# Kernel tuning notes

Hardware: AMD Instinct MI355X
Metric: run time of the kernel (lower is better)

The kernel has to match this reference:

```python
import jax, jax.numpy as jnp
import numpy as np

H = 1024  # hidden_size
I = 1     # input_size / output_size


def _lstm_cell(x_t, h, c, Wih, Whh, b):
    # PyTorch gate order: i, f, g, o ; Wih:[4H,I], Whh:[4H,H], b:[4H]
    gates = x_t @ Wih.T + h @ Whh.T + b          # [B, 4H]
    i, f, g, o = jnp.split(gates, 4, axis=-1)
    c_new = jax.nn.sigmoid(f) * c + jax.nn.sigmoid(i) * jnp.tanh(g)
    h_new = jax.nn.sigmoid(o) * jnp.tanh(c_new)
    return h_new, c_new


def setup_inputs() -> dict:
    key = jax.random.key(0)
    ks = jax.random.split(key, 10)
    s = 1.0 / np.sqrt(H)
    u = lambda k, shp: jax.random.uniform(k, shp, jnp.float32, -s, s)
    seq_len, batch = 512, 512
    return {
        "x": jax.random.normal(ks[0], (seq_len, batch, I), jnp.float32),
        "enc_Wih": u(ks[1], (4 * H, I)),
        "enc_Whh": u(ks[2], (4 * H, H)),
        "enc_b": u(ks[3], (4 * H,)),
        "dec_Wih": u(ks[4], (4 * H, I)),
        "dec_Whh": u(ks[5], (4 * H, H)),
        "dec_b": u(ks[6], (4 * H,)),
        "lin_W": u(ks[7], (I, H)),
        "lin_b": u(ks[8], (I,)),
        "target_len": 64,
    }


def reference(x, enc_Wih, enc_Whh, enc_b, dec_Wih, dec_Whh, dec_b, lin_W, lin_b, target_len):
    batch = x.shape[1]
    h0 = jnp.zeros((batch, H), x.dtype)
    c0 = jnp.zeros((batch, H), x.dtype)

    # Encoder: single LSTM over the full sequence; only final (h, c) is used.
    def enc_step(carry, x_t):
        h, c = carry
        h, c = _lstm_cell(x_t, h, c, enc_Wih, enc_Whh, enc_b)
        return (h, c), None

    (h, c), _ = jax.lax.scan(enc_step, (h0, c0), x)

    # Recursive decoder: feed own output back as next input.
    def dec_step(carry, _):
        h, c, y_in = carry
        h, c = _lstm_cell(y_in, h, c, dec_Wih, dec_Whh, dec_b)
        y = h @ lin_W.T + lin_b                  # [B, I]
        return (h, c, y), y

    dec_in0 = x[-1]                              # [B, I]
    _, y = jax.lax.scan(dec_step, (h, c, dec_in0), None, length=target_len)
    return y                                      # [target_len, B, I]
```

## Files before the change

kernel.cpp:

```cpp
#include <hip/hip_runtime.h>
#include <cstdint>
#include <cstddef>


#define HD    1024
#define G4    4096
#define NSTEP 576
#define TLEN  64

typedef __bf16 bf16x8 __attribute__((ext_vector_type(8)));
typedef float  f32x4  __attribute__((ext_vector_type(4)));
typedef __attribute__((address_space(1))) const unsigned int glob_u32;
typedef __attribute__((address_space(3))) unsigned int lds_u32;

__device__ __forceinline__ unsigned short f2bf(float f) {
  unsigned u = __builtin_bit_cast(unsigned, f);
  u = u + 0x7FFFu + ((u >> 16) & 1u);
  return (unsigned short)(u >> 16);
}
__device__ __forceinline__ float bf2f(unsigned short h) {
  return __builtin_bit_cast(float, (unsigned)h << 16);
}
__device__ __forceinline__ float sigm(float x) { return 1.0f / (1.0f + __expf(-x)); }
__device__ __forceinline__ float tanh_(float x) { return 1.0f - 2.0f / (1.0f + __expf(2.0f * x)); }

__global__ __launch_bounds__(256) void prep_w(const float* __restrict__ Whh,
                                              const float* __restrict__ Wih,
                                              const float* __restrict__ linW,
                                              int fold,
                                              unsigned short* __restrict__ dst) {
  int gid  = blockIdx.x * 256 + threadIdx.x;
  int rowg = gid >> 8;
  int k0   = (gid & 255) << 2;
  float4 wv = *reinterpret_cast<const float4*>(Whh + (size_t)rowg * HD + k0);
  if (fold) {
    float wi = Wih[rowg];
    float4 lw = *reinterpret_cast<const float4*>(linW + k0);
    wv.x += wi * lw.x; wv.y += wi * lw.y; wv.z += wi * lw.z; wv.w += wi * lw.w;
  }
  ushort4 hi, lo;
  hi.x = f2bf(wv.x); lo.x = f2bf(wv.x - bf2f(hi.x));
  hi.y = f2bf(wv.y); lo.y = f2bf(wv.y - bf2f(hi.y));
  hi.z = f2bf(wv.z); lo.z = f2bf(wv.z - bf2f(hi.z));
  hi.w = f2bf(wv.w); lo.w = f2bf(wv.w - bf2f(hi.w));
  int g = rowg >> 10, j = rowg & 1023;
  int tile = j >> 3, c = g * 8 + (j & 7);
  size_t base = (size_t)tile * 65536 + (size_t)c * 1024 + (size_t)(k0 ^ ((c & 7) << 3));
  *reinterpret_cast<ushort4*>(dst + base)         = hi;
  *reinterpret_cast<ushort4*>(dst + base + 32768) = lo;
}

__global__ __launch_bounds__(256) void init_out(float* __restrict__ out,
                                                const float* __restrict__ lin_b) {
  int i = blockIdx.x * 256 + threadIdx.x;
  if (i < TLEN * 512) out[i] = lin_b[0];
}

__global__ __launch_bounds__(512, 1) void lstm_step(
    const float* __restrict__ xv,
    const float* __restrict__ psub,
    const float* __restrict__ xcp,
    const float* __restrict__ Wih,
    const float* __restrict__ bias,
    const float* __restrict__ linW,
    const unsigned short* __restrict__ wbuf,
    const unsigned short* __restrict__ hT_in,
    unsigned short* __restrict__ hT_out,
    float* __restrict__ c_buf,
    float* __restrict__ yout)
{
  __shared__ __align__(16) unsigned char smem[131072 + 512];
  const int tid  = threadIdx.x;
  const int lane = tid & 63;
  const int wid  = tid >> 6;
  const int l15  = lane & 15;
  const int lk   = lane >> 4;

  const int bid  = blockIdx.x;
  const int rh   = (bid >> 2) & 1;
  const int tile = (bid >> 3) * 4 + (bid & 3);

  {
    glob_u32* g = (glob_u32*)(wbuf + (size_t)tile * 65536);
    lds_u32*  l = (lds_u32*)smem;
#pragma unroll
    for (int i = 0; i < 16; ++i)
      __builtin_amdgcn_global_load_lds(g + i * 2048 + tid * 4,
                                       l + i * 2048 + tid * 4, 16, 0, 0);
  }
  float* wihs = (float*)(smem + 131072);
  float* bs   = (float*)(smem + 131072 + 128);
  float* lws  = (float*)(smem + 131072 + 256);
  if (tid < 32) {
    int g = tid >> 3, jj = tid & 7;
    int r = g * HD + tile * 8 + jj;
    wihs[tid] = Wih[r];
    bs[tid]   = bias[r];
  } else if (tid < 40) {
    lws[tid - 32] = linW[tile * 8 + (tid - 32)];
  }
  __syncthreads();

  const int rowbase = rh * 256 + wid * 32;
  const unsigned short* pa[2];
#pragma unroll
  for (int m = 0; m < 2; ++m)
    pa[m] = hT_in + (size_t)(rowbase + m * 16 + l15) * 32 + lk * 8;

  int QH[2], QL[2];
#pragma unroll
  for (int nt = 0; nt < 2; ++nt) {
    int c = nt * 16 + l15;
    int s = (c & 7) << 4;
    int q = c * 2048 + ((lk * 16) ^ s);
    QH[nt] = q;
    QL[nt] = 65536 + q;
  }

  f32x4 acc[2][2] = {};
  bf16x8 Af[3][2], BH[2][2], BL[2][2];

#define LOADA(kk, st)                                                        \
  { _Pragma("unroll") for (int m = 0; m < 2; ++m)                            \
      Af[st][m] = *(const bf16x8*)(pa[m] + (size_t)(kk) * 16384); }
#define LOADB(kk, st)                                                        \
  { _Pragma("unroll") for (int nt = 0; nt < 2; ++nt) {                       \
      BH[st][nt] = *(const bf16x8*)(smem + (QH[nt] ^ ((kk) << 6)));          \
      BL[st][nt] = *(const bf16x8*)(smem + (QL[nt] ^ ((kk) << 6))); } }

  LOADA(0, 0); LOADA(1, 1); LOADB(0, 0);
#pragma unroll
  for (int kk = 0; kk < 32; ++kk) {
    if (kk + 2 < 32) LOADA(kk + 2, (kk + 2) % 3);
    if (kk + 1 < 32) LOADB(kk + 1, (kk + 1) & 1);
#pragma unroll
    for (int m = 0; m < 2; ++m)
#pragma unroll
      for (int nt = 0; nt < 2; ++nt) {
        acc[m][nt] = __builtin_amdgcn_mfma_f32_16x16x32_bf16(
            Af[kk % 3][m], BH[kk & 1][nt], acc[m][nt], 0, 0, 0);
        acc[m][nt] = __builtin_amdgcn_mfma_f32_16x16x32_bf16(
            Af[kk % 3][m], BL[kk & 1][nt], acc[m][nt], 0, 0, 0);
      }
  }
#undef LOADA
#undef LOADB

  __syncthreads();
  float* gl = (float*)smem;
#pragma unroll
  for (int m = 0; m < 2; ++m)
#pragma unroll
    for (int nt = 0; nt < 2; ++nt)
#pragma unroll
      for (int r = 0; r < 4; ++r)
        gl[(wid * 32 + m * 16 + lk * 4 + r) * 33 + nt * 16 + l15] = acc[m][nt][r];
  __syncthreads();

  const int row  = tid >> 1;
  const int jp   = tid & 1;
  const int grow = rh * 256 + row;
  float xs = 0.0f;
  if (xv)   xs += xv[grow];
  if (psub) xs -= psub[grow];
  if (xcp)  xs += xcp[0];

  float* cp = c_buf + (size_t)tile * 4096 + rh * 2048 + row * 8 + jp * 4;
  float4 cold = *reinterpret_cast<const float4*>(cp);
  float4 cnew;
  ushort4 hw;
  float ypart = 0.0f;
#pragma unroll
  for (int q = 0; q < 4; ++q) {
    int jj = jp * 4 + q;
    float gi = gl[row * 33 + jj]      + xs * wihs[jj]      + bs[jj];
    float gf = gl[row * 33 + 8 + jj]  + xs * wihs[8 + jj]  + bs[8 + jj];
    float gg = gl[row * 33 + 16 + jj] + xs * wihs[16 + jj] + bs[16 + jj];
    float go = gl[row * 33 + 24 + jj] + xs * wihs[24 + jj] + bs[24 + jj];
    float cv = (&cold.x)[q];
    float cn = sigm(gf) * cv + sigm(gi) * tanh_(gg);
    float hn = sigm(go) * tanh_(cn);
    (&cnew.x)[q] = cn;
    ypart += hn * lws[jj];
    ((unsigned short*)&hw)[q] = f2bf(hn);
  }
  *reinterpret_cast<float4*>(cp) = cnew;
  const int kblk = tile >> 2;
  const int keb  = (tile & 3) * 8;
  *reinterpret_cast<ushort4*>(hT_out + (size_t)kblk * 16384 + (size_t)grow * 32
                              + keb + jp * 4) = hw;
  if (yout) {
    ypart += __shfl_xor(ypart, 1);
    if ((lane & 1) == 0) atomicAdd(yout + grow, ypart);
  }
}

extern "C" void kernel_launch(void* const* d_in, const int* in_sizes, int n_in,
                              void* d_out, int out_size, void* d_ws, size_t ws_size,
                              hipStream_t stream) {
  const float* x       = (const float*)d_in[0];
  const float* enc_Wih = (const float*)d_in[1];
  const float* enc_Whh = (const float*)d_in[2];
  const float* enc_b   = (const float*)d_in[3];
  const float* dec_Wih = (const float*)d_in[4];
  const float* dec_Whh = (const float*)d_in[5];
  const float* dec_b   = (const float*)d_in[6];
  const float* lin_W   = (const float*)d_in[7];
  const float* lin_b   = (const float*)d_in[8];
  float* out = (float*)d_out;

  uint8_t* w = (uint8_t*)d_ws;
  const size_t MB = 1u << 20;
  float*          c_buf = (float*)(w + 0 * MB);
  unsigned short* hT0   = (unsigned short*)(w + 2 * MB);
  float*          p     = (float*)(w + 3 * MB);
  unsigned short* hT1   = (unsigned short*)(w + 4 * MB);
  unsigned short* wenc  = (unsigned short*)(w + 8 * MB);
  unsigned short* wdec  = (unsigned short*)(w + 24 * MB);
  unsigned short* hT[2] = { hT0, hT1 };

  hipMemsetAsync(d_ws, 0, 3 * MB + 4096, stream);
  init_out<<<128, 256, 0, stream>>>(out, lin_b);
  prep_w<<<4096, 256, 0, stream>>>(enc_Whh, enc_Wih, lin_W, 0, wenc);
  prep_w<<<4096, 256, 0, stream>>>(dec_Whh, dec_Wih, lin_W, 1, wdec);

  for (int t = 0; t < NSTEP; ++t) {
    const unsigned short* hin = hT[t & 1];
    unsigned short* hout      = hT[(t + 1) & 1];
    if (t < 512) {
      lstm_step<<<256, 512, 0, stream>>>(
          x + (size_t)t * 512, nullptr, nullptr,
          enc_Wih, enc_b, lin_W, wenc, hin, hout, c_buf,
          (t == 511) ? p : nullptr);
    } else if (t == 512) {
      lstm_step<<<256, 512, 0, stream>>>(
          x + (size_t)511 * 512, p, nullptr,
          dec_Wih, dec_b, lin_W, wdec, hin, hout, c_buf, out);
    } else {
      int s = t - 512;
      lstm_step<<<256, 512, 0, stream>>>(
          nullptr, nullptr, lin_b,
          dec_Wih, dec_b, lin_W, wdec, hin, hout, c_buf,
          out + (size_t)s * 512);
    }
  }
  (void)in_sizes; (void)n_in; (void)out_size; (void)ws_size;
}
```

Baseline: 11.79 ms.

## Replace per-step kernel launches with a persistent kernel using grid barriers

```diff
diff --git a/kernel.cpp b/kernel.cpp
--- a/kernel.cpp
+++ b/kernel.cpp
@@ -56,20 +56,28 @@
   if (i < TLEN * 512) out[i] = lin_b[0];
 }
 
-__global__ __launch_bounds__(512, 1) void lstm_step(
-    const float* __restrict__ xv,
-    const float* __restrict__ psub,
-    const float* __restrict__ xcp,
-    const float* __restrict__ Wih,
-    const float* __restrict__ bias,
+__global__ __launch_bounds__(512, 1) void lstm_persist(
+    const float* __restrict__ x,
+    const float* __restrict__ enc_Wih,
+    const float* __restrict__ enc_b,
+    const float* __restrict__ dec_Wih,
+    const float* __restrict__ dec_b,
     const float* __restrict__ linW,
-    const unsigned short* __restrict__ wbuf,
-    const unsigned short* __restrict__ hT_in,
-    unsigned short* __restrict__ hT_out,
-    float* __restrict__ c_buf,
-    float* __restrict__ yout)
+    const float* __restrict__ linb_p,
+    const unsigned short* __restrict__ wenc,
+    const unsigned short* __restrict__ wdec,
+    unsigned short* __restrict__ hA,
+    unsigned short* __restrict__ hB,
+    float* __restrict__ p,
+    unsigned* __restrict__ bar,
+    float* __restrict__ out)
 {
-  __shared__ __align__(16) unsigned char smem[131072 + 512];
+  __shared__ __align__(16) unsigned char smem[148480];
+  float* gl   = (float*)(smem + 131072);
+  float* wihs = (float*)(smem + 131072 + 16896);
+  float* bs   = wihs + 32;
+  float* lws  = wihs + 64;
+
   const int tid  = threadIdx.x;
   const int lane = tid & 63;
   const int wid  = tid >> 6;
@@ -79,33 +87,15 @@
   const int bid  = blockIdx.x;
   const int rh   = (bid >> 2) & 1;
   const int tile = (bid >> 3) * 4 + (bid & 3);
-
-  {
-    glob_u32* g = (glob_u32*)(wbuf + (size_t)tile * 65536);
-    lds_u32*  l = (lds_u32*)smem;
-#pragma unroll
-    for (int i = 0; i < 16; ++i)
-      __builtin_amdgcn_global_load_lds(g + i * 2048 + tid * 4,
-                                       l + i * 2048 + tid * 4, 16, 0, 0);
-  }
-  float* wihs = (float*)(smem + 131072);
-  float* bs   = (float*)(smem + 131072 + 128);
-  float* lws  = (float*)(smem + 131072 + 256);
-  if (tid < 32) {
-    int g = tid >> 3, jj = tid & 7;
-    int r = g * HD + tile * 8 + jj;
-    wihs[tid] = Wih[r];
-    bs[tid]   = bias[r];
-  } else if (tid < 40) {
-    lws[tid - 32] = linW[tile * 8 + (tid - 32)];
-  }
-  __syncthreads();
+  const int kblk = tile >> 2;
+  const float linb = linb_p[0];
+  unsigned* cnt = bar + rh * 32;
 
   const int rowbase = rh * 256 + wid * 32;
-  const unsigned short* pa[2];
+  size_t aoff[2];
 #pragma unroll
   for (int m = 0; m < 2; ++m)
-    pa[m] = hT_in + (size_t)(rowbase + m * 16 + l15) * 32 + lk * 8;
+    aoff[m] = (size_t)(rowbase + m * 16 + l15) * 32 + (size_t)lk * 8;
 
   int QH[2], QL[2];
 #pragma unroll
@@ -117,8 +107,47 @@
     QL[nt] = 65536 + q;
   }
 
-  f32x4 acc[2][2] = {};
-  bf16x8 Af[3][2], BH[2][2], BL[2][2];
+  const int rowc = tid >> 2;
+  const int jq   = tid & 3;
+
+  float c_reg[2][2] = {{0.f, 0.f}, {0.f, 0.f}};
+
+#define STAGE(WB, WIH, BB)                                                   \
+  {                                                                          \
+    glob_u32* gsrc = (glob_u32*)((WB) + (size_t)tile * 65536);               \
+    lds_u32*  ldst = (lds_u32*)smem;                                         \
+    _Pragma("unroll")                                                        \
+    for (int i = 0; i < 16; ++i)                                             \
+      __builtin_amdgcn_global_load_lds(gsrc + i * 2048 + tid * 4,            \
+                                       ldst + i * 2048 + tid * 4, 16, 0, 0); \
+    if (tid < 32) {                                                          \
+      int gg = tid >> 3, jj = tid & 7;                                       \
+      int r = gg * HD + tile * 8 + jj;                                       \
+      wihs[tid] = (WIH)[r];                                                  \
+      bs[tid]   = (BB)[r];                                                   \
+    } else if (tid < 40) {                                                   \
+      lws[tid - 32] = linW[tile * 8 + (tid - 32)];                           \
+    }                                                                        \
+  }
+
+  STAGE(wenc, enc_Wih, enc_b);
+  __syncthreads();
+
+#pragma unroll 1
+  for (int t = 0; t < NSTEP; ++t) {
+    if (t == 512) {
+      STAGE(wdec, dec_Wih, dec_b);
+      __syncthreads();
+    }
+    const unsigned short* hin = (t & 1) ? hB : hA;
+    unsigned short* hout      = (t & 1) ? hA : hB;
+
+    const unsigned short* pa[2];
+#pragma unroll
+    for (int m = 0; m < 2; ++m) pa[m] = hin + aoff[m];
+
+    f32x4 acc[2][2] = {};
+    bf16x8 Af[3][2], BH[2][2], BL[2][2];
 
 #define LOADA(kk, st)                                                        \
   { _Pragma("unroll") for (int m = 0; m < 2; ++m)                            \
@@ -128,71 +157,83 @@
       BH[st][nt] = *(const bf16x8*)(smem + (QH[nt] ^ ((kk) << 6)));          \
       BL[st][nt] = *(const bf16x8*)(smem + (QL[nt] ^ ((kk) << 6))); } }
 
-  LOADA(0, 0); LOADA(1, 1); LOADB(0, 0);
-#pragma unroll
-  for (int kk = 0; kk < 32; ++kk) {
-    if (kk + 2 < 32) LOADA(kk + 2, (kk + 2) % 3);
-    if (kk + 1 < 32) LOADB(kk + 1, (kk + 1) & 1);
-#pragma unroll
-    for (int m = 0; m < 2; ++m)
-#pragma unroll
-      for (int nt = 0; nt < 2; ++nt) {
-        acc[m][nt] = __builtin_amdgcn_mfma_f32_16x16x32_bf16(
-            Af[kk % 3][m], BH[kk & 1][nt], acc[m][nt], 0, 0, 0);
-        acc[m][nt] = __builtin_amdgcn_mfma_f32_16x16x32_bf16(
-            Af[kk % 3][m], BL[kk & 1][nt], acc[m][nt], 0, 0, 0);
-      }
-  }
+    LOADA(0, 0); LOADA(1, 1); LOADB(0, 0);
+#pragma unroll
+    for (int kk = 0; kk < 32; ++kk) {
+      if (kk + 2 < 32) LOADA(kk + 2, (kk + 2) % 3);
+      if (kk + 1 < 32) LOADB(kk + 1, (kk + 1) & 1);
+#pragma unroll
+      for (int m = 0; m < 2; ++m)
+#pragma unroll
+        for (int nt = 0; nt < 2; ++nt) {
+          acc[m][nt] = __builtin_amdgcn_mfma_f32_16x16x32_bf16(
+              Af[kk % 3][m], BH[kk & 1][nt], acc[m][nt], 0, 0, 0);
+          acc[m][nt] = __builtin_amdgcn_mfma_f32_16x16x32_bf16(
+              Af[kk % 3][m], BL[kk & 1][nt], acc[m][nt], 0, 0, 0);
+        }
+    }
 #undef LOADA
 #undef LOADB
 
-  __syncthreads();
-  float* gl = (float*)smem;
-#pragma unroll
-  for (int m = 0; m < 2; ++m)
-#pragma unroll
-    for (int nt = 0; nt < 2; ++nt)
-#pragma unroll
-      for (int r = 0; r < 4; ++r)
-        gl[(wid * 32 + m * 16 + lk * 4 + r) * 33 + nt * 16 + l15] = acc[m][nt][r];
-  __syncthreads();
-
-  const int row  = tid >> 1;
-  const int jp   = tid & 1;
-  const int grow = rh * 256 + row;
-  float xs = 0.0f;
-  if (xv)   xs += xv[grow];
-  if (psub) xs -= psub[grow];
-  if (xcp)  xs += xcp[0];
-
-  float* cp = c_buf + (size_t)tile * 4096 + rh * 2048 + row * 8 + jp * 4;
-  float4 cold = *reinterpret_cast<const float4*>(cp);
-  float4 cnew;
-  ushort4 hw;
-  float ypart = 0.0f;
-#pragma unroll
-  for (int q = 0; q < 4; ++q) {
-    int jj = jp * 4 + q;
-    float gi = gl[row * 33 + jj]      + xs * wihs[jj]      + bs[jj];
-    float gf = gl[row * 33 + 8 + jj]  + xs * wihs[8 + jj]  + bs[8 + jj];
-    float gg = gl[row * 33 + 16 + jj] + xs * wihs[16 + jj] + bs[16 + jj];
-    float go = gl[row * 33 + 24 + jj] + xs * wihs[24 + jj] + bs[24 + jj];
-    float cv = (&cold.x)[q];
-    float cn = sigm(gf) * cv + sigm(gi) * tanh_(gg);
-    float hn = sigm(go) * tanh_(cn);
-    (&cnew.x)[q] = cn;
-    ypart += hn * lws[jj];
-    ((unsigned short*)&hw)[q] = f2bf(hn);
-  }
-  *reinterpret_cast<float4*>(cp) = cnew;
-  const int kblk = tile >> 2;
-  const int keb  = (tile & 3) * 8;
-  *reinterpret_cast<ushort4*>(hT_out + (size_t)kblk * 16384 + (size_t)grow * 32
-                              + keb + jp * 4) = hw;
-  if (yout) {
-    ypart += __shfl_xor(ypart, 1);
-    if ((lane & 1) == 0) atomicAdd(yout + grow, ypart);
-  }
+#pragma unroll
+    for (int half = 0; half < 2; ++half) {
+      __syncthreads();
+#pragma unroll
+      for (int nt = 0; nt < 2; ++nt)
+#pragma unroll
+        for (int r = 0; r < 4; ++r)
+          gl[(wid * 16 + lk * 4 + r) * 33 + nt * 16 + l15] = acc[half][nt][r];
+      __syncthreads();
+
+      const int grow = rh * 256 + ((rowc >> 4) << 5) + half * 16 + (rowc & 15);
+      float xs;
+      if (t < 512)       xs = x[(size_t)t * 512 + grow];
+      else if (t == 512) xs = x[(size_t)511 * 512 + grow] - p[grow];
+      else               xs = linb;
+
+      float yp = 0.0f;
+      unsigned short hw[2];
+#pragma unroll
+      for (int q = 0; q < 2; ++q) {
+        int jj = jq * 2 + q;
+        float gi = gl[rowc * 33 + jj]      + xs * wihs[jj]      + bs[jj];
+        float gf = gl[rowc * 33 + 8 + jj]  + xs * wihs[8 + jj]  + bs[8 + jj];
+        float gg = gl[rowc * 33 + 16 + jj] + xs * wihs[16 + jj] + bs[16 + jj];
+        float go = gl[rowc * 33 + 24 + jj] + xs * wihs[24 + jj] + bs[24 + jj];
+        float cn = sigm(gf) * c_reg[half][q] + sigm(gi) * tanh_(gg);
+        c_reg[half][q] = cn;
+        float hn = sigm(go) * tanh_(cn);
+        yp += hn * lws[jj];
+        hw[q] = f2bf(hn);
+      }
+      *reinterpret_cast<ushort2*>(hout + (size_t)kblk * 16384 + (size_t)grow * 32
+                                  + (tile & 3) * 8 + jq * 2)
+          = *reinterpret_cast<ushort2*>(hw);
+      if (t >= 511) {
+        yp += __shfl_xor(yp, 1);
+        yp += __shfl_xor(yp, 2);
+        if (jq == 0) {
+          if (t == 511) atomicAdd(p + grow, yp);
+          else          atomicAdd(out + (size_t)(t - 512) * 512 + grow, yp);
+        }
+      }
+    }
+
+    if (t != NSTEP - 1) {
+      __syncthreads();
+      if (tid == 0) {
+        __threadfence();
+        atomicAdd(cnt, 1u);
+        unsigned tgt = (unsigned)(t + 1) * 128u;
+        while (__hip_atomic_load(cnt, __ATOMIC_RELAXED,
+                                 __HIP_MEMORY_SCOPE_AGENT) < tgt)
+          __builtin_amdgcn_s_sleep(2);
+        __threadfence();
+      }
+      __syncthreads();
+    }
+  }
+#undef STAGE
 }
 
 extern "C" void kernel_launch(void* const* d_in, const int* in_sizes, int n_in,
@@ -211,38 +252,22 @@
 
   uint8_t* w = (uint8_t*)d_ws;
   const size_t MB = 1u << 20;
-  float*          c_buf = (float*)(w + 0 * MB);
-  unsigned short* hT0   = (unsigned short*)(w + 2 * MB);
-  float*          p     = (float*)(w + 3 * MB);
-  unsigned short* hT1   = (unsigned short*)(w + 4 * MB);
-  unsigned short* wenc  = (unsigned short*)(w + 8 * MB);
-  unsigned short* wdec  = (unsigned short*)(w + 24 * MB);
-  unsigned short* hT[2] = { hT0, hT1 };
-
-  hipMemsetAsync(d_ws, 0, 3 * MB + 4096, stream);
+  unsigned short* hA   = (unsigned short*)(w + 0 * MB);
+  unsigned short* hB   = (unsigned short*)(w + 1 * MB);
+  float*          p    = (float*)(w + 2 * MB);
+  unsigned*       bar  = (unsigned*)(w + 2 * MB + 4096);
+  unsigned short* wenc = (unsigned short*)(w + 4 * MB);
+  unsigned short* wdec = (unsigned short*)(w + 20 * MB);
+
+  hipMemsetAsync(hA, 0, MB, stream);
+  hipMemsetAsync(p, 0, 8192, stream);
   init_out<<<128, 256, 0, stream>>>(out, lin_b);
   prep_w<<<4096, 256, 0, stream>>>(enc_Whh, enc_Wih, lin_W, 0, wenc);
   prep_w<<<4096, 256, 0, stream>>>(dec_Whh, dec_Wih, lin_W, 1, wdec);
 
-  for (int t = 0; t < NSTEP; ++t) {
-    const unsigned short* hin = hT[t & 1];
-    unsigned short* hout      = hT[(t + 1) & 1];
-    if (t < 512) {
-      lstm_step<<<256, 512, 0, stream>>>(
-          x + (size_t)t * 512, nullptr, nullptr,
-          enc_Wih, enc_b, lin_W, wenc, hin, hout, c_buf,
-          (t == 511) ? p : nullptr);
-    } else if (t == 512) {
-      lstm_step<<<256, 512, 0, stream>>>(
-          x + (size_t)511 * 512, p, nullptr,
-          dec_Wih, dec_b, lin_W, wdec, hin, hout, c_buf, out);
-    } else {
-      int s = t - 512;
-      lstm_step<<<256, 512, 0, stream>>>(
-          nullptr, nullptr, lin_b,
-          dec_Wih, dec_b, lin_W, wdec, hin, hout, c_buf,
-          out + (size_t)s * 512);
-    }
-  }
+  lstm_persist<<<256, 512, 0, stream>>>(
+      x, enc_Wih, enc_b, dec_Wih, dec_b, lin_W, lin_b,
+      wenc, wdec, hA, hB, p, bar, out);
+
   (void)in_sizes; (void)n_in; (void)out_size; (void)ws_size;
 }
```

Measured after the change: 15.40 ms. 1.31x slower.
